# Kernel tuning notes

Measured on AMD Instinct MI355X. Metric: run time of the kernel, lower is better.

The kernel has to match this reference:

```python
import jax, jax.numpy as jnp
import numpy as np

H, D = 8, 16
HID = H * D  # hidden_channels = 128
SQRT_D = float(np.sqrt(D))


def setup_inputs() -> dict:
    key = jax.random.key(0)
    ks = iter(jax.random.split(key, 64))
    def nrm(shape, scale):
        return jax.random.normal(next(ks), shape, dtype=jnp.float32) * scale
    def rint(n, hi):
        return jax.random.randint(next(ks), (n,), 0, hi, dtype=jnp.int32)
    E = 250000
    Nh, Ni, Nt = 8000, 40000, 20000
    inp = {
        'x_herb': nrm((Nh, 400), 1.0),
        'x_ing':  nrm((Ni, 300), 1.0),
        'x_tgt':  nrm((Nt, 200), 1.0),
        # per-type input projections
        'W_herb': nrm((400, HID), 0.05), 'b_herb': jnp.zeros((HID,), jnp.float32),
        'W_ing':  nrm((300, HID), 0.06), 'b_ing':  jnp.zeros((HID,), jnp.float32),
        'W_tgt':  nrm((200, HID), 0.07), 'b_tgt':  jnp.zeros((HID,), jnp.float32),
        # HGTConv per-node-type k/q/v linears, stacked over [herb, ing, tgt]
        'Wk': nrm((3, HID, HID), 0.09), 'bk': jnp.zeros((3, HID), jnp.float32),
        'Wq': nrm((3, HID, HID), 0.09), 'bq': jnp.zeros((3, HID), jnp.float32),
        'Wv': nrm((3, HID, HID), 0.09), 'bv': jnp.zeros((3, HID), jnp.float32),
        # per-edge-type relation matrices / priors, stacked over 4 edge types
        'a_rel': nrm((4, H, D, D), 0.25),
        'm_rel': nrm((4, H, D, D), 0.25),
        'p_rel': jnp.ones((4, H), jnp.float32),
        # per-dst-node-type output linear + skip gate
        'Wa': nrm((3, HID, HID), 0.09), 'ba': jnp.zeros((3, HID), jnp.float32),
        'skip': jnp.ones((3,), jnp.float32),
        # final herb linear
        'W_out': nrm((HID, HID), 0.09), 'b_out': jnp.zeros((HID,), jnp.float32),
        # edge lists: (herb->ing contains), (ing->herb rev), (ing->tgt targets), (tgt->ing rev)
        'src_ci': rint(E, Nh), 'dst_ci': rint(E, Ni),
        'src_ic': rint(E, Ni), 'dst_ic': rint(E, Nh),
        'src_it': rint(E, Ni), 'dst_it': rint(E, Nt),
        'src_ti': rint(E, Nt), 'dst_ti': rint(E, Ni),
    }
    return inp


def _hetero_forward(x_herb, x_ing, x_tgt, W_herb, b_herb, W_ing, b_ing, W_tgt, b_tgt,
                    Wk, bk, Wq, bq, Wv, bv, a_rel, m_rel, p_rel, Wa, ba, skip,
                    W_out, b_out, src_ci, dst_ci, src_ic, dst_ic, src_it, dst_it,
                    src_ti, dst_ti):
    types = ['herb', 'ing', 'tgt']
    xs = {'herb': x_herb @ W_herb + b_herb,
          'ing':  x_ing  @ W_ing  + b_ing,
          'tgt':  x_tgt  @ W_tgt  + b_tgt}
    Ns = {t: xs[t].shape[0] for t in types}
    # per-node-type k/q/v, reshaped to [N, H, D]
    k = {t: (xs[t] @ Wk[i] + bk[i]).reshape(-1, H, D) for i, t in enumerate(types)}
    q = {t: (xs[t] @ Wq[i] + bq[i]).reshape(-1, H, D) for i, t in enumerate(types)}
    v = {t: (xs[t] @ Wv[i] + bv[i]).reshape(-1, H, D) for i, t in enumerate(types)}

    edge_defs = [  # (edge_type_id, src_type, dst_type, src_idx, dst_idx)
        (0, 'herb', 'ing', src_ci, dst_ci),
        (1, 'ing', 'herb', src_ic, dst_ic),
        (2, 'ing', 'tgt', src_it, dst_it),
        (3, 'tgt', 'ing', src_ti, dst_ti),
    ]
    contrib = {t: [] for t in types}
    for e, s, t, src, dst in edge_defs:
        # relation-specific transforms at node level, then gather per edge
        k_rel = jnp.einsum('nhd,hde->nhe', k[s], a_rel[e])  # [Ns, H, D]
        v_rel = jnp.einsum('nhd,hde->nhe', v[s], m_rel[e])  # [Ns, H, D]
        logit = (q[t][dst] * k_rel[src]).sum(-1) * (p_rel[e] / SQRT_D)  # [E, H]
        contrib[t].append((logit, v_rel[src], dst))

    out = {}
    for i, t in enumerate(types):
        logits = jnp.concatenate([c[0] for c in contrib[t]], axis=0)  # [Et, H]
        msgs = jnp.concatenate([c[1] for c in contrib[t]], axis=0)    # [Et, H, D]
        dsts = jnp.concatenate([c[2] for c in contrib[t]], axis=0)    # [Et]
        n = Ns[t]
        # segment softmax over all incoming edges of each dst node (per head)
        mx = jax.ops.segment_max(logits, dsts, num_segments=n)
        ex = jnp.exp(logits - mx[dsts])
        den = jax.ops.segment_sum(ex, dsts, num_segments=n)
        alpha = ex / (den[dsts] + 1e-16)
        agg = jax.ops.segment_sum(msgs * alpha[:, :, None], dsts, num_segments=n)
        agg = agg.reshape(n, HID)
        o = jax.nn.gelu(agg, approximate=False) @ Wa[i] + ba[i]
        g = jax.nn.sigmoid(skip[i])
        out[t] = jax.nn.relu(g * o + (1.0 - g) * xs[t])
    out_herb = out['herb'] @ W_out + b_out
    return (out_herb, out['ing'], out['tgt'])


def reference(x_herb, x_ing, x_tgt, W_herb, b_herb, W_ing, b_ing, W_tgt, b_tgt,
              Wk, bk, Wq, bq, Wv, bv, a_rel, m_rel, p_rel, Wa, ba, skip,
              W_out, b_out, src_ci, dst_ci, src_ic, dst_ic, src_it, dst_it,
              src_ti, dst_ti):
    return _hetero_forward(x_herb, x_ing, x_tgt, W_herb, b_herb, W_ing, b_ing,
                           W_tgt, b_tgt, Wk, bk, Wq, bq, Wv, bv, a_rel, m_rel,
                           p_rel, Wa, ba, skip, W_out, b_out, src_ci, dst_ci,
                           src_ic, dst_ic, src_it, dst_it, src_ti, dst_ti)
```

## Files before the change

### kernel.cpp

```cpp
#include <hip/hip_runtime.h>
#include <math.h>

#define HID 128
typedef unsigned int uint;
typedef unsigned short ushort;
typedef __attribute__((ext_vector_type(8))) short short8;
typedef __attribute__((ext_vector_type(4))) float floatx4;
typedef __attribute__((ext_vector_type(2))) float f32x2;

__device__ __forceinline__ ushort f2b(float f) {
  uint u = __float_as_uint(f);
  u += 0x7fffu + ((u >> 16) & 1u);
  return (ushort)(u >> 16);
}
__device__ __forceinline__ float b2f(ushort s) {
  return __uint_as_float(((uint)s) << 16);
}
__device__ __forceinline__ float blo(uint u) { return __uint_as_float(u << 16); }
__device__ __forceinline__ float bhi(uint u) { return __uint_as_float(u & 0xffff0000u); }
__device__ __forceinline__ f32x2 b2x2(uint u) {
  f32x2 r;
  r.x = __uint_as_float(u << 16);
  r.y = __uint_as_float(u & 0xffff0000u);
  return r;
}

__device__ __forceinline__ void gll16(const ushort* g, ushort* l) {
  __builtin_amdgcn_global_load_lds(
      (const __attribute__((address_space(1))) void*)g,
      (__attribute__((address_space(3))) void*)l, 16, 0, 0);
}

__device__ __forceinline__ size_t a_packed_us(int rr, int col) {
  int tm = rr >> 7, prow = rr & 127;
  int ptk = col >> 5, kin = col & 31;
  int sw = (kin >> 3) ^ ((prow >> 1) & 3);
  return (((size_t)tm * 4 + ptk) * 512 + (size_t)prow * 4 + sw) * 8 + (kin & 7);
}

struct PackSeg { const float* X; ushort* out; int M, K, Ktiles, start; };
struct WBlk { const float* src; ushort* dst; int K; int start; };
struct Prolog {
  PackSeg pk[3];
  int crwstart, wstart, bstart, total;
  const float *Wk, *bk, *Wv, *bv, *a_rel, *m_rel, *p_rel;
  ushort* kw_dst[4];
  ushort* vw_dst[4];
  float* bcat;
  int kb_off[4], vb_off[4];
  WBlk wb[10];
  const float* bq;
  int bq_off[3];
};

__device__ void combine_rel_elem(const Prolog& P, int idx)
{
  int col  = idx & 127;
  int rest = idx >> 7;
  int row  = rest % 129;
  rest /= 129;
  int kv = rest & 1;
  int e  = rest >> 1;
  int i  = (e + 1) >> 1;
  int h = col >> 4, j = col & 15;
  const float* Wsrc = kv ? P.Wv : P.Wk;
  const float* bsrc = kv ? P.bv : P.bk;
  const float* rel  = kv ? P.m_rel : P.a_rel;
  float acc = 0.f;
  if (row < 128) {
#pragma unroll
    for (int d = 0; d < 16; ++d)
      acc += Wsrc[(size_t)i * 16384 + (size_t)row * 128 + h * 16 + d] *
             rel[((e * 8 + h) * 16 + d) * 16 + j];
  } else {
#pragma unroll
    for (int d = 0; d < 16; ++d)
      acc += bsrc[i * 128 + h * 16 + d] * rel[((e * 8 + h) * 16 + d) * 16 + j];
  }
  if (!kv) acc *= P.p_rel[e * 8 + h] * 0.36067376022224085f;
  if (row < 128) {
    ushort* dst = kv ? P.vw_dst[e] : P.kw_dst[e];
    int tk = row >> 5, chunk = (row >> 3) & 3, m = row & 7;
    int swf = chunk ^ ((col >> 1) & 3);
    dst[((tk * 512 + col * 4 + swf) << 3) + m] = f2b(acc);
  } else {
    P.bcat[(kv ? P.vb_off[e] : P.kb_off[e]) + col] = acc;
  }
}

__device__ void conv_elem(const Prolog& P, int s0)
{
  int si = 0;
#pragma unroll
  for (int k = 1; k < 10; ++k)
    if (s0 >= P.wb[k].start) si = k;
  WBlk b = P.wb[si];
  int s = s0 - b.start;
  int tk = s >> 9, o = s & 511;
  int c = o >> 2, swf = o & 3;
  int chunk = swf ^ ((c >> 1) & 3);
  int r0 = tk * 32 + chunk * 8;
  ushort tmp[8];
#pragma unroll
  for (int m = 0; m < 8; ++m) {
    int r = r0 + m;
    tmp[m] = (r < b.K) ? f2b(b.src[(size_t)r * 128 + c]) : (ushort)0;
  }
  *(short8*)&b.dst[(size_t)s * 8] = *(short8*)tmp;
}

__global__ __launch_bounds__(256)
void prologue(Prolog P)
{
  int gtid = blockIdx.x * 256 + threadIdx.x;
  if (gtid >= P.total) return;
  if (gtid >= P.bstart) {
    int j = gtid - P.bstart;
    P.bcat[P.bq_off[j >> 7] + (j & 127)] = P.bq[j];
    return;
  }
  if (gtid >= P.wstart) { conv_elem(P, gtid - P.wstart); return; }
  if (gtid >= P.crwstart) { combine_rel_elem(P, gtid - P.crwstart); return; }
  int si = 0;
  if (gtid >= P.pk[2].start) si = 2;
  else if (gtid >= P.pk[1].start) si = 1;
  const PackSeg s = P.pk[si];
  int slot = gtid - s.start;
  int spm = s.Ktiles << 9;
  int tm = slot / spm, r2 = slot - tm * spm;
  int tk = r2 >> 9, o = r2 & 511;
  int row = o >> 2, sw = o & 3;
  int chunk = sw ^ ((row >> 1) & 3);
  int grow = tm * 128 + row;
  int gk = tk * 32 + chunk * 8;
  ushort tmp[8];
  if (grow < s.M && gk + 8 <= s.K) {
    const float* p = s.X + (size_t)grow * s.K + gk;
    float4 a = *(const float4*)p, b = *(const float4*)(p + 4);
    tmp[0] = f2b(a.x); tmp[1] = f2b(a.y); tmp[2] = f2b(a.z); tmp[3] = f2b(a.w);
    tmp[4] = f2b(b.x); tmp[5] = f2b(b.y); tmp[6] = f2b(b.z); tmp[7] = f2b(b.w);
  } else {
#pragma unroll
    for (int j = 0; j < 8; ++j) {
      int kk = gk + j;
      tmp[j] = (grow < s.M && kk < s.K) ? f2b(s.X[(size_t)grow * s.K + kk]) : (ushort)0;
    }
  }
  *(short8*)&s.out[(size_t)slot * 8] = *(short8*)tmp;
}

#define CSR_CH 1024
#define CSR_SH 9

struct EdgeStreams {
  const int* src[4]; const int* dst[4];
  int off[4]; uint rel[4]; uint ldb[4];
};

__global__ __launch_bounds__(256)
void edge_hist(EdgeStreams es, uint* __restrict__ hist, int NBs, int NBK, int E)
{
  __shared__ uint h[512];
  int b = blockIdx.x;
  int et = b / NBs;
  int i0 = (b - et * NBs) * CSR_CH;
  const int* dp = es.dst[et];
  int off = es.off[et];
  for (int t = threadIdx.x; t < NBK; t += 256) h[t] = 0;
  __syncthreads();
#pragma unroll
  for (int j = 0; j < CSR_CH / 256; ++j) {
    int idx = i0 + j * 256 + threadIdx.x;
    if (idx < E) atomicAdd(&h[(uint)(off + dp[idx]) >> CSR_SH], 1u);
  }
  __syncthreads();
  for (int t = threadIdx.x; t < NBK; t += 256)
    hist[(size_t)b * NBK + t] = h[t];
}

__global__ __launch_bounds__(256)
void bucket_scan(uint* __restrict__ hist, uint* __restrict__ bucketTot,
                 int NBlk, int NBK)
{
  __shared__ uint ws[4];
  __shared__ uint carry_s;
  int b = blockIdx.x;
  int t = threadIdx.x, lane = t & 63, w = t >> 6;
  if (t == 0) carry_s = 0;
  __syncthreads();
  for (int base = 0; base < NBlk; base += 256) {
    int i = base + t;
    uint x = (i < NBlk) ? hist[(size_t)i * NBK + b] : 0u;
    uint v = x;
#pragma unroll
    for (int o = 1; o < 64; o <<= 1) {
      uint y = __shfl_up(v, o, 64);
      if (lane >= o) v += y;
    }
    if (lane == 63) ws[w] = v;
    __syncthreads();
    uint add = carry_s;
    for (int k = 0; k < w; ++k) add += ws[k];
    if (i < NBlk) hist[(size_t)i * NBK + b] = add + v - x;
    __syncthreads();
    if (t == 255) carry_s = add + v;
    __syncthreads();
  }
  if (t == 0) bucketTot[b] = carry_s;
}

__global__ __launch_bounds__(256)
void bucket_base(const uint* __restrict__ bucketTot, uint* __restrict__ bucketBase,
                 int NBK, int* __restrict__ starts, int Ntot)
{
  __shared__ uint ws[4];
  __shared__ uint carry_s;
  int t = threadIdx.x, lane = t & 63, w = t >> 6;
  if (t == 0) carry_s = 0;
  __syncthreads();
  for (int base = 0; base < NBK; base += 256) {
    int i = base + t;
    uint x = (i < NBK) ? bucketTot[i] : 0u;
    uint v = x;
#pragma unroll
    for (int o = 1; o < 64; o <<= 1) {
      uint y = __shfl_up(v, o, 64);
      if (lane >= o) v += y;
    }
    if (lane == 63) ws[w] = v;
    __syncthreads();
    uint add = carry_s;
    for (int k = 0; k < w; ++k) add += ws[k];
    if (i < NBK) bucketBase[i] = add + v - x;
    __syncthreads();
    if (t == 255) carry_s = add + v;
    __syncthreads();
  }
  if (t == 0) { bucketBase[NBK] = carry_s; starts[Ntot] = (int)carry_s; }
}

__global__ __launch_bounds__(256)
void bucket_scatter(EdgeStreams es, const uint* __restrict__ hist,
                    const uint* __restrict__ bucketBase,
                    uint2* __restrict__ inter, int NBs, int NBK, int E)
{
  __shared__ uint cur[512];
  int b = blockIdx.x;
  int et = b / NBs;
  int i0 = (b - et * NBs) * CSR_CH;
  const int* dp = es.dst[et];
  const int* sp = es.src[et];
  int off = es.off[et];
  uint rel = es.rel[et], ldb = es.ldb[et];
  for (int t = threadIdx.x; t < NBK; t += 256)
    cur[t] = bucketBase[t] + hist[(size_t)b * NBK + t];
  __syncthreads();
#pragma unroll
  for (int j = 0; j < CSR_CH / 256; ++j) {
    int idx = i0 + j * 256 + threadIdx.x;
    if (idx < E) {
      int g = off + dp[idx];
      uint pos = atomicAdd(&cur[(uint)g >> CSR_SH], 1u);
      inter[pos] = make_uint2(rel + (uint)sp[idx] * ldb, (uint)g);
    }
  }
}

__global__ __launch_bounds__(256)
void bucket_finalize(const uint2* __restrict__ inter,
                     const uint* __restrict__ bucketBase,
                     int* __restrict__ starts, uint* __restrict__ payload, int Ntot)
{
  __shared__ uint ncnt[512];
  __shared__ uint ws[4];
  int b = blockIdx.x;
  int g0 = b << CSR_SH;
  int t = threadIdx.x, lane = t & 63, w = t >> 6;
  uint r0 = bucketBase[b], r1 = bucketBase[b + 1];
  ncnt[t] = 0; ncnt[t + 256] = 0;
  __syncthreads();
  for (uint i = r0 + t; i < r1; i += 256)
    atomicAdd(&ncnt[inter[i].y - g0], 1u);
  __syncthreads();
  uint a0 = ncnt[2 * t], a1 = ncnt[2 * t + 1];
  uint s = a0 + a1;
  uint v = s;
#pragma unroll
  for (int o = 1; o < 64; o <<= 1) {
    uint y = __shfl_up(v, o, 64);
    if (lane >= o) v += y;
  }
  if (lane == 63) ws[w] = v;
  __syncthreads();
  uint add = r0;
  for (int k = 0; k < w; ++k) add += ws[k];
  uint e0 = add + v - s;
  int gi = g0 + 2 * t;
  if (gi < Ntot)     starts[gi]     = (int)e0;
  if (gi + 1 < Ntot) starts[gi + 1] = (int)(e0 + a0);
  ncnt[2 * t] = e0;
  ncnt[2 * t + 1] = e0 + a0;
  __syncthreads();
  for (uint i = r0 + t; i < r1; i += 256) {
    uint2 rec = inter[i];
    uint pos = atomicAdd(&ncnt[rec.y - g0], 1u);
    payload[pos] = rec.x;
  }
}

struct GemmSeg {
  const ushort* A; const ushort* B; const float* bias;
  void* out; const ushort* xsP;
  int Ktiles, ldo, Mreal, skip_idx, epi, NT, start;
};
struct Gemm3 { GemmSeg s[3]; const float* skip; int nseg; };

__launch_bounds__(256)
__global__ void gemm_sched(Gemm3 g3)
{
  __shared__ __align__(16) ushort As[2][4096];
  __shared__ __align__(16) ushort Bs[2][4096];
  int bid = blockIdx.x;
  int si = 0;
  if (g3.nseg > 1 && bid >= g3.s[1].start)
    si = (g3.nseg > 2 && bid >= g3.s[2].start) ? 2 : 1;
  const GemmSeg sg = g3.s[si];
  int local = bid - sg.start;
  int tm = local / sg.NT, tn = local - tm * sg.NT;

  const int t = threadIdx.x;
  const int wave = t >> 6, lane = t & 63;
  const int wm = (wave >> 1) * 64, wn = (wave & 1) * 64;
  const int l16 = lane & 15, quad = lane >> 4;
  const int Ktiles = sg.Ktiles;

  const ushort* Abase = sg.A + (size_t)tm * Ktiles * 4096;
  const ushort* Bbase = sg.B + (size_t)tn * Ktiles * 4096;

  floatx4 acc[4][4];
#pragma unroll
  for (int i = 0; i < 4; ++i)
#pragma unroll
    for (int j = 0; j < 4; ++j) acc[i][j] = (floatx4){0.f, 0.f, 0.f, 0.f};

  auto stage = [&](int tk, int buf) {
#pragma unroll
    for (int j = 0; j < 4; ++j) {
      int c = wave * 4 + j;
      if (c < 8)
        gll16(Abase + (size_t)tk * 4096 + c * 512 + lane * 8, &As[buf][c * 512]);
      else
        gll16(Bbase + (size_t)tk * 4096 + (c - 8) * 512 + lane * 8, &Bs[buf][(c - 8) * 512]);
    }
  };

  stage(0, 0);
  __syncthreads();

  for (int tk = 0; tk < Ktiles; ++tk) {
    int buf = tk & 1;
    if (tk + 1 < Ktiles) stage(tk + 1, buf ^ 1);

    short8 af[4], bfr[4];
    const int swz = (quad ^ ((l16 >> 1) & 3)) * 8;
#pragma unroll
    for (int i = 0; i < 4; ++i) {
      af[i]  = *(const short8*)&As[buf][(wm + i * 16 + l16) * 32 + swz];
      bfr[i] = *(const short8*)&Bs[buf][(wn + i * 16 + l16) * 32 + swz];
    }
#pragma unroll
    for (int mi = 0; mi < 4; ++mi)
#pragma unroll
      for (int ni = 0; ni < 4; ++ni)
        acc[mi][ni] = __builtin_amdgcn_mfma_f32_16x16x32_bf16(
            af[mi], bfr[ni], acc[mi][ni], 0, 0, 0);
    __syncthreads();
  }

  const int epi = sg.epi;
  float g = 0.f, omg = 0.f;
  if (epi == 2 || epi == 3) {
    float s = g3.skip[sg.skip_idx];
    g = 1.f / (1.f + __expf(-s));
    omg = 1.f - g;
  }
#pragma unroll
  for (int ni = 0; ni < 4; ++ni) {
    int col = tn * 128 + wn + ni * 16 + l16;
    float bb = sg.bias[col];
#pragma unroll
    for (int mi = 0; mi < 4; ++mi) {
      int rloc = wm + mi * 16 + quad * 4;
#pragma unroll
      for (int r = 0; r < 4; ++r) {
        int prow = rloc + r;
        int rr = tm * 128 + prow;
        float v = acc[mi][ni][r] + bb;
        if (epi == 0) {
          ((ushort*)sg.out)[(size_t)rr * sg.ldo + col] = f2b(v);
        } else if (epi == 1) {
          if (rr < sg.Mreal) ((float*)sg.out)[(size_t)rr * sg.ldo + col] = v;
        } else if (epi == 2) {
          if (rr < sg.Mreal) {
            float xo = b2f(sg.xsP[a_packed_us(rr, col)]);
            ((float*)sg.out)[(size_t)rr * sg.ldo + col] = fmaxf(g * v + omg * xo, 0.f);
          }
        } else if (epi == 3) {
          float xo = b2f(sg.xsP[a_packed_us(rr, col)]);
          ((ushort*)sg.out)[a_packed_us(rr, col)] = f2b(fmaxf(g * v + omg * xo, 0.f));
        } else {
          ((ushort*)sg.out)[a_packed_us(rr, col)] = f2b(v);
        }
      }
    }
  }
}

struct GatherType { const ushort* q; ushort* agg; int ldq; };
struct GatherDesc { GatherType ty[3]; int n0, n1; };

__launch_bounds__(256)
__global__ void gather_all(const int* __restrict__ starts,
                           const uint* __restrict__ payload,
                           const ushort* __restrict__ kvbase,
                           GatherDesc gd, int Ntot)
{
  int wid = (blockIdx.x * 256 + threadIdx.x) >> 6;
  if (wid >= Ntot) return;
  int lane = threadIdx.x & 63;
  int g = lane >> 4, l = lane & 15;

  GatherType T;
  int d;
  if (wid < gd.n0)      { T = gd.ty[0]; d = wid; }
  else if (wid < gd.n1) { T = gd.ty[1]; d = wid - gd.n0; }
  else                  { T = gd.ty[2]; d = wid - gd.n1; }

  const char* kvb = (const char*)kvbase;
  const uint lofs = (uint)l * 16u;

  uint4 qv = *(const uint4*)(T.q + (size_t)d * T.ldq + l * 8);
  f32x2 q0 = b2x2(qv.x), q1 = b2x2(qv.y), q2 = b2x2(qv.z), q3 = b2x2(qv.w);

  int e0 = starts[wid], e1 = starts[wid + 1];
  float lsum = 0.f;
  f32x2 ac0 = {0.f, 0.f}, ac1 = {0.f, 0.f}, ac2 = {0.f, 0.f}, ac3 = {0.f, 0.f};

  for (int eb = e0; eb < e1; eb += 8) {
    int eA = eb + g, eB = eA + 4;
    bool actA = eA < e1, actB = eB < e1;
    uint pA = payload[actA ? eA : e0];
    uint pB = payload[actB ? eB : e0];
    const char* bA = kvb + (pA + lofs);
    const char* bB = kvb + (pB + lofs);
    uint4 kA = *(const uint4*)bA;
    uint4 vA = *(const uint4*)(bA + 256);
    uint4 kB = *(const uint4*)bB;
    uint4 vB = *(const uint4*)(bB + 256);

    f32x2 dA = q0 * b2x2(kA.x);
    dA = __builtin_elementwise_fma(q1, b2x2(kA.y), dA);
    dA = __builtin_elementwise_fma(q2, b2x2(kA.z), dA);
    dA = __builtin_elementwise_fma(q3, b2x2(kA.w), dA);
    f32x2 dB = q0 * b2x2(kB.x);
    dB = __builtin_elementwise_fma(q1, b2x2(kB.y), dB);
    dB = __builtin_elementwise_fma(q2, b2x2(kB.z), dB);
    dB = __builtin_elementwise_fma(q3, b2x2(kB.w), dB);
    float pa = dA.x + dA.y;
    float pb = dB.x + dB.y;
    pa += __shfl_xor(pa, 1, 64);
    pb += __shfl_xor(pb, 1, 64);
    float exA = exp2f(fminf(pa, 115.4f));
    float exB = exp2f(fminf(pb, 115.4f));
    exA = actA ? exA : 0.f;
    exB = actB ? exB : 0.f;
    lsum += exA + exB;
    f32x2 xA = {exA, exA}, xB = {exB, exB};
    ac0 = __builtin_elementwise_fma(xA, b2x2(vA.x), ac0);
    ac1 = __builtin_elementwise_fma(xA, b2x2(vA.y), ac1);
    ac2 = __builtin_elementwise_fma(xA, b2x2(vA.z), ac2);
    ac3 = __builtin_elementwise_fma(xA, b2x2(vA.w), ac3);
    ac0 = __builtin_elementwise_fma(xB, b2x2(vB.x), ac0);
    ac1 = __builtin_elementwise_fma(xB, b2x2(vB.y), ac1);
    ac2 = __builtin_elementwise_fma(xB, b2x2(vB.z), ac2);
    ac3 = __builtin_elementwise_fma(xB, b2x2(vB.w), ac3);
  }

  float s0 = ac0.x, s1 = ac0.y, s2 = ac1.x, s3 = ac1.y;
  float s4 = ac2.x, s5 = ac2.y, s6 = ac3.x, s7 = ac3.y;
#define MRG(v) v += __shfl_xor(v, 16, 64); v += __shfl_xor(v, 32, 64)
  MRG(lsum); MRG(s0); MRG(s1); MRG(s2); MRG(s3); MRG(s4); MRG(s5); MRG(s6); MRG(s7);
#undef MRG

  float inv = 1.f / (lsum + 1e-16f);
  float m0 = (g & 1) ? s2 : s0, m1 = (g & 1) ? s6 : s4;
  float n0 = (g & 1) ? s3 : s1, n1 = (g & 1) ? s7 : s5;
  float x0 = ((g & 2) ? m1 : m0) * inv;
  float x1 = ((g & 2) ? n1 : n0) * inv;
  float g0 = 0.5f * x0 * (1.f + erff(x0 * 0.70710678118654752f));
  float g1 = 0.5f * x1 * (1.f + erff(x1 * 0.70710678118654752f));
  int tm = d >> 7, row = d & 127;
  int tk = l >> 2, sw = (l & 3) ^ ((row >> 1) & 3);
  size_t us = (((size_t)tm * 4 + tk) * 512 + (size_t)row * 4 + sw) * 8 + 2 * g;
  *(uint*)(T.agg + us) = ((uint)f2b(g1) << 16) | (uint)f2b(g0);
}

extern "C" void kernel_launch(void* const* d_in, const int* in_sizes, int n_in,
                              void* d_out, int out_size, void* d_ws, size_t ws_size,
                              hipStream_t stream)
{
  const float* x_herb = (const float*)d_in[0];
  const float* x_ing  = (const float*)d_in[1];
  const float* x_tgt  = (const float*)d_in[2];
  const float* W_herb = (const float*)d_in[3];
  const float* b_herb = (const float*)d_in[4];
  const float* W_ing  = (const float*)d_in[5];
  const float* b_ing  = (const float*)d_in[6];
  const float* W_tgt  = (const float*)d_in[7];
  const float* b_tgt  = (const float*)d_in[8];
  const float* Wk     = (const float*)d_in[9];
  const float* bk     = (const float*)d_in[10];
  const float* Wq     = (const float*)d_in[11];
  const float* bq     = (const float*)d_in[12];
  const float* Wv     = (const float*)d_in[13];
  const float* bv     = (const float*)d_in[14];
  const float* a_rel  = (const float*)d_in[15];
  const float* m_rel  = (const float*)d_in[16];
  const float* p_rel  = (const float*)d_in[17];
  const float* Wa     = (const float*)d_in[18];
  const float* ba     = (const float*)d_in[19];
  const float* skip   = (const float*)d_in[20];
  const float* W_out  = (const float*)d_in[21];
  const float* b_out  = (const float*)d_in[22];
  const int* srcs[4] = {(const int*)d_in[23], (const int*)d_in[25],
                        (const int*)d_in[27], (const int*)d_in[29]};
  const int* dsts[4] = {(const int*)d_in[24], (const int*)d_in[26],
                        (const int*)d_in[28], (const int*)d_in[30]};

  const int Nh = in_sizes[0] / 400;
  const int Ni = in_sizes[1] / 300;
  const int Nt = in_sizes[2] / 200;
  const int E  = in_sizes[23];
  const int Ntot = Nh + Ni + Nt;

  const int MT_h = (Nh + 127) / 128, MT_i = (Ni + 127) / 128, MT_t = (Nt + 127) / 128;
  const int KT_h = 13, KT_i = 10, KT_t = 7;

  const int NBs = (E + CSR_CH - 1) / CSR_CH;
  const int NBlk = 4 * NBs;
  const int NBK = (Ntot + (1 << CSR_SH) - 1) >> CSR_SH;

  char* base = (char*)d_ws;
  size_t off = 0;
  auto A = [&](size_t bytes) -> void* {
    void* p = base + off; off += (bytes + 255) & ~(size_t)255; return p;
  };
  ushort* xp_h  = (ushort*)A((size_t)MT_h * KT_h * 8192);
  ushort* xp_i  = (ushort*)A((size_t)MT_i * KT_i * 8192);
  ushort* xp_t  = (ushort*)A((size_t)MT_t * KT_t * 8192);
  ushort* xsP_h = (ushort*)A((size_t)MT_h * 4 * 8192);
  ushort* xsP_i = (ushort*)A((size_t)MT_i * 4 * 8192);
  ushort* xsP_t = (ushort*)A((size_t)MT_t * 4 * 8192);
  ushort* fused_h = (ushort*)A((size_t)MT_h * 128 * 384 * 2);
  ushort* fused_i = (ushort*)A((size_t)MT_i * 128 * 640 * 2);
  ushort* fused_t = (ushort*)A((size_t)MT_t * 128 * 384 * 2);
  ushort* aggp_h  = (ushort*)A((size_t)MT_h * 4 * 8192);
  ushort* aggp_i  = (ushort*)A((size_t)MT_i * 4 * 8192);
  ushort* aggp_t  = (ushort*)A((size_t)MT_t * 4 * 8192);
  ushort* htmp_p  = (ushort*)A((size_t)MT_h * 4 * 8192);
  ushort* Weff1_h = (ushort*)A((size_t)KT_h * 8192);
  ushort* Weff1_i = (ushort*)A((size_t)KT_i * 8192);
  ushort* Weff1_t = (ushort*)A((size_t)KT_t * 8192);
  ushort* Wcat_h = (ushort*)A((size_t)3 * 4 * 8192);
  ushort* Wcat_i = (ushort*)A((size_t)5 * 4 * 8192);
  ushort* Wcat_t = (ushort*)A((size_t)3 * 4 * 8192);
  float* bcat   = (float*)A(1408 * 4);
  ushort* Wa_t   = (ushort*)A((size_t)3 * 16384 * 2);
  ushort* Wout_t = (ushort*)A((size_t)16384 * 2);
  int* starts  = (int*)A((size_t)(Ntot + 4) * 4);
  uint* payload = (uint*)A((size_t)(4 * E + 8) * 4);
  uint* hist    = (uint*)A((size_t)NBlk * NBK * 4);
  uint* bucketTot  = (uint*)A((size_t)NBK * 4);
  uint* bucketBase = (uint*)A((size_t)(NBK + 1) * 4);
  uint2* inter  = (uint2*)A((size_t)(4 * E + 8) * 8);
  (void)ws_size; (void)n_in;

  const int toff_h = 0, toff_i = Nh, toff_t = Nh + Ni;
  dim3 blk(256);

  int sl_h = MT_h * KT_h * 512, sl_i = MT_i * KT_i * 512, sl_t = MT_t * KT_t * 512;
  Prolog P;
  P.pk[0] = {x_herb, xp_h, Nh, 400, KT_h, 0};
  P.pk[1] = {x_ing,  xp_i, Ni, 300, KT_i, sl_h};
  P.pk[2] = {x_tgt,  xp_t, Nt, 200, KT_t, sl_h + sl_i};
  P.crwstart = sl_h + sl_i + sl_t;
  P.wstart = P.crwstart + 4 * 2 * 129 * 128;
  {
    const float* wsrc10[10] = {W_herb, W_ing, W_tgt, Wq, Wq + 16384, Wq + 32768,
                               Wa, Wa + 16384, Wa + 32768, W_out};
    ushort* wdst10[10] = {Weff1_h, Weff1_i, Weff1_t, Wcat_h, Wcat_i, Wcat_t,
                          Wa_t, Wa_t + 16384, Wa_t + 32768, Wout_t};
    int wk10[10] = {400, 300, 200, 128, 128, 128, 128, 128, 128, 128};
    int wcum = 0;
    for (int z = 0; z < 10; ++z) {
      P.wb[z] = {wsrc10[z], wdst10[z], wk10[z], wcum};
      wcum += ((wk10[z] + 31) / 32) * 512;
    }
    P.bstart = P.wstart + wcum;
  }
  P.total = P.bstart + 384;
  P.Wk = Wk; P.bk = bk; P.Wv = Wv; P.bv = bv;
  P.a_rel = a_rel; P.m_rel = m_rel; P.p_rel = p_rel;
  P.kw_dst[0] = Wcat_h + 16384; P.vw_dst[0] = Wcat_h + 32768;
  P.kw_dst[1] = Wcat_i + 16384; P.vw_dst[1] = Wcat_i + 32768;
  P.kw_dst[2] = Wcat_i + 49152; P.vw_dst[2] = Wcat_i + 65536;
  P.kw_dst[3] = Wcat_t + 16384; P.vw_dst[3] = Wcat_t + 32768;
  P.bcat = bcat;
  P.kb_off[0] = 128;  P.vb_off[0] = 256;
  P.kb_off[1] = 512;  P.vb_off[1] = 640;
  P.kb_off[2] = 768;  P.vb_off[2] = 896;
  P.kb_off[3] = 1152; P.vb_off[3] = 1280;
  P.bq = bq;
  P.bq_off[0] = 0; P.bq_off[1] = 384; P.bq_off[2] = 1024;
  prologue<<<(P.total + 255) / 256, blk, 0, stream>>>(P);

  uint fi2 = (uint)((size_t)(fused_i - fused_h) * 2);
  uint ft2 = (uint)((size_t)(fused_t - fused_h) * 2);
  EdgeStreams ES;
  ES.src[0] = srcs[0]; ES.dst[0] = dsts[0]; ES.off[0] = toff_i;
  ES.rel[0] = 256u;        ES.ldb[0] = 768u;
  ES.src[1] = srcs[1]; ES.dst[1] = dsts[1]; ES.off[1] = toff_h;
  ES.rel[1] = fi2 + 256u;  ES.ldb[1] = 1280u;
  ES.src[2] = srcs[2]; ES.dst[2] = dsts[2]; ES.off[2] = toff_t;
  ES.rel[2] = fi2 + 768u;  ES.ldb[2] = 1280u;
  ES.src[3] = srcs[3]; ES.dst[3] = dsts[3]; ES.off[3] = toff_i;
  ES.rel[3] = ft2 + 256u;  ES.ldb[3] = 768u;
  edge_hist<<<NBlk, blk, 0, stream>>>(ES, hist, NBs, NBK, E);
  bucket_scan<<<NBK, blk, 0, stream>>>(hist, bucketTot, NBlk, NBK);
  bucket_base<<<1, blk, 0, stream>>>(bucketTot, bucketBase, NBK, starts, Ntot);
  bucket_scatter<<<NBlk, blk, 0, stream>>>(ES, hist, bucketBase, inter, NBs, NBK, E);
  bucket_finalize<<<NBK, blk, 0, stream>>>(inter, bucketBase, starts, payload, Ntot);

  Gemm3 G1;
  G1.skip = skip; G1.nseg = 3;
  G1.s[0] = {xp_h, Weff1_h, b_herb, xsP_h, nullptr, KT_h, 0, 0, 0, 4, 1, 0};
  G1.s[1] = {xp_i, Weff1_i, b_ing,  xsP_i, nullptr, KT_i, 0, 0, 0, 4, 1, MT_h};
  G1.s[2] = {xp_t, Weff1_t, b_tgt,  xsP_t, nullptr, KT_t, 0, 0, 0, 4, 1, MT_h + MT_i};
  gemm_sched<<<MT_h + MT_i + MT_t, blk, 0, stream>>>(G1);

  Gemm3 G2;
  G2.skip = skip; G2.nseg = 3;
  G2.s[0] = {xsP_h, Wcat_h, bcat + 0,    fused_h, nullptr, 4, 384, 0, 0, 0, 3, 0};
  G2.s[1] = {xsP_i, Wcat_i, bcat + 384,  fused_i, nullptr, 4, 640, 0, 0, 0, 5, MT_h * 3};
  G2.s[2] = {xsP_t, Wcat_t, bcat + 1024, fused_t, nullptr, 4, 384, 0, 0, 0, 3,
             MT_h * 3 + MT_i * 5};
  gemm_sched<<<MT_h * 3 + MT_i * 5 + MT_t * 3, blk, 0, stream>>>(G2);

  GatherDesc GD;
  GD.n0 = Nh; GD.n1 = Nh + Ni;
  GD.ty[0] = {fused_h, aggp_h, 384};
  GD.ty[1] = {fused_i, aggp_i, 640};
  GD.ty[2] = {fused_t, aggp_t, 384};
  gather_all<<<(Ntot + 3) / 4, blk, 0, stream>>>(starts, payload, fused_h, GD, Ntot);

  float* outp = (float*)d_out;
  float* out_herb = outp;
  float* out_ing  = outp + (size_t)Nh * HID;
  float* out_tgt  = outp + (size_t)(Nh + Ni) * HID;
  Gemm3 GE;
  GE.skip = skip; GE.nseg = 3;
  GE.s[0] = {aggp_h, Wa_t + 0 * 16384, ba + 0 * 128, htmp_p, xsP_h,
             4, 0, 0, 0, 3, 1, 0};
  GE.s[1] = {aggp_i, Wa_t + 1 * 16384, ba + 1 * 128, out_ing, xsP_i,
             4, 128, Ni, 1, 2, 1, MT_h};
  GE.s[2] = {aggp_t, Wa_t + 2 * 16384, ba + 2 * 128, out_tgt, xsP_t,
             4, 128, Nt, 2, 2, 1, MT_h + MT_i};
  gemm_sched<<<MT_h + MT_i + MT_t, blk, 0, stream>>>(GE);

  Gemm3 GF;
  GF.skip = skip; GF.nseg = 1;
  GF.s[0] = {htmp_p, Wout_t, b_out, out_herb, nullptr, 4, 128, Nh, 0, 1, 1, 0};
  GF.s[1] = GF.s[0]; GF.s[2] = GF.s[0];
  gemm_sched<<<MT_h, blk, 0, stream>>>(GF);
  (void)out_size;
}
```

Before: 456.4 us.

## Fold edge histogram into prologue, drop bucket_base kernel, unroll gather loop

```diff
diff --git a/kernel.cpp b/kernel.cpp
--- a/kernel.cpp
+++ b/kernel.cpp
@@ -37,6 +37,14 @@
   int sw = (kin >> 3) ^ ((prow >> 1) & 3);
   return (((size_t)tm * 4 + ptk) * 512 + (size_t)prow * 4 + sw) * 8 + (kin & 7);
 }
+
+#define CSR_CH 2048
+#define CSR_SH 9
+
+struct EdgeStreams {
+  const int* src[4]; const int* dst[4];
+  int off[4]; uint rel[4]; uint ldb[4];
+};
 
 struct PackSeg { const float* X; ushort* out; int M, K, Ktiles, start; };
 struct WBlk { const float* src; ushort* dst; int K; int start; };
@@ -51,6 +59,10 @@
   WBlk wb[10];
   const float* bq;
   int bq_off[3];
+  const int* edst[4];
+  int eoff[4];
+  uint* hist;
+  int NBs, NBH, NBK, E;
 };
 
 __device__ void combine_rel_elem(const Prolog& P, int idx)
@@ -112,7 +124,26 @@
 __global__ __launch_bounds__(256)
 void prologue(Prolog P)
 {
-  int gtid = blockIdx.x * 256 + threadIdx.x;
+  __shared__ uint h[512];
+  int bI = blockIdx.x;
+  if (bI < P.NBH) {
+    int et = bI / P.NBs;
+    int i0 = (bI - et * P.NBs) * CSR_CH;
+    const int* dp = P.edst[et];
+    int off = P.eoff[et];
+    for (int t = threadIdx.x; t < P.NBK; t += 256) h[t] = 0;
+    __syncthreads();
+#pragma unroll
+    for (int j = 0; j < CSR_CH / 256; ++j) {
+      int idx = i0 + j * 256 + threadIdx.x;
+      if (idx < P.E) atomicAdd(&h[(uint)(off + dp[idx]) >> CSR_SH], 1u);
+    }
+    __syncthreads();
+    for (int t = threadIdx.x; t < P.NBK; t += 256)
+      P.hist[(size_t)t * P.NBH + bI] = h[t];
+    return;
+  }
+  int gtid = (bI - P.NBH) * 256 + threadIdx.x;
   if (gtid >= P.total) return;
   if (gtid >= P.bstart) {
     int j = gtid - P.bstart;
@@ -149,38 +180,8 @@
   *(short8*)&s.out[(size_t)slot * 8] = *(short8*)tmp;
 }
 
-#define CSR_CH 1024
-#define CSR_SH 9
-
-struct EdgeStreams {
-  const int* src[4]; const int* dst[4];
-  int off[4]; uint rel[4]; uint ldb[4];
-};
-
 __global__ __launch_bounds__(256)
-void edge_hist(EdgeStreams es, uint* __restrict__ hist, int NBs, int NBK, int E)
-{
-  __shared__ uint h[512];
-  int b = blockIdx.x;
-  int et = b / NBs;
-  int i0 = (b - et * NBs) * CSR_CH;
-  const int* dp = es.dst[et];
-  int off = es.off[et];
-  for (int t = threadIdx.x; t < NBK; t += 256) h[t] = 0;
-  __syncthreads();
-#pragma unroll
-  for (int j = 0; j < CSR_CH / 256; ++j) {
-    int idx = i0 + j * 256 + threadIdx.x;
-    if (idx < E) atomicAdd(&h[(uint)(off + dp[idx]) >> CSR_SH], 1u);
-  }
-  __syncthreads();
-  for (int t = threadIdx.x; t < NBK; t += 256)
-    hist[(size_t)b * NBK + t] = h[t];
-}
-
-__global__ __launch_bounds__(256)
-void bucket_scan(uint* __restrict__ hist, uint* __restrict__ bucketTot,
-                 int NBlk, int NBK)
+void bucket_scan(uint* __restrict__ hist, uint* __restrict__ bucketTot, int NBH)
 {
   __shared__ uint ws[4];
   __shared__ uint carry_s;
@@ -188,9 +189,9 @@
   int t = threadIdx.x, lane = t & 63, w = t >> 6;
   if (t == 0) carry_s = 0;
   __syncthreads();
-  for (int base = 0; base < NBlk; base += 256) {
+  for (int base = 0; base < NBH; base += 256) {
     int i = base + t;
-    uint x = (i < NBlk) ? hist[(size_t)i * NBK + b] : 0u;
+    uint x = (i < NBH) ? hist[(size_t)b * NBH + i] : 0u;
     uint v = x;
 #pragma unroll
     for (int o = 1; o < 64; o <<= 1) {
@@ -201,7 +202,7 @@
     __syncthreads();
     uint add = carry_s;
     for (int k = 0; k < w; ++k) add += ws[k];
-    if (i < NBlk) hist[(size_t)i * NBK + b] = add + v - x;
+    if (i < NBH) hist[(size_t)b * NBH + i] = add + v - x;
     __syncthreads();
     if (t == 255) carry_s = add + v;
     __syncthreads();
@@ -209,42 +210,40 @@
   if (t == 0) bucketTot[b] = carry_s;
 }
 
-__global__ __launch_bounds__(256)
-void bucket_base(const uint* __restrict__ bucketTot, uint* __restrict__ bucketBase,
-                 int NBK, int* __restrict__ starts, int Ntot)
-{
-  __shared__ uint ws[4];
-  __shared__ uint carry_s;
+__device__ __forceinline__ void base_scan(const uint* __restrict__ bucketTot,
+                                          uint* sb, uint* ws, int NBK)
+{
   int t = threadIdx.x, lane = t & 63, w = t >> 6;
-  if (t == 0) carry_s = 0;
-  __syncthreads();
-  for (int base = 0; base < NBK; base += 256) {
-    int i = base + t;
-    uint x = (i < NBK) ? bucketTot[i] : 0u;
-    uint v = x;
-#pragma unroll
-    for (int o = 1; o < 64; o <<= 1) {
-      uint y = __shfl_up(v, o, 64);
-      if (lane >= o) v += y;
-    }
-    if (lane == 63) ws[w] = v;
-    __syncthreads();
-    uint add = carry_s;
-    for (int k = 0; k < w; ++k) add += ws[k];
-    if (i < NBK) bucketBase[i] = add + v - x;
-    __syncthreads();
-    if (t == 255) carry_s = add + v;
-    __syncthreads();
-  }
-  if (t == 0) { bucketBase[NBK] = carry_s; starts[Ntot] = (int)carry_s; }
+  sb[t] = (t < NBK) ? bucketTot[t] : 0u;
+  sb[t + 256] = (t + 256 < NBK) ? bucketTot[t + 256] : 0u;
+  __syncthreads();
+  uint a0 = sb[2 * t], a1 = sb[2 * t + 1];
+  uint s = a0 + a1;
+  uint v = s;
+#pragma unroll
+  for (int o = 1; o < 64; o <<= 1) {
+    uint y = __shfl_up(v, o, 64);
+    if (lane >= o) v += y;
+  }
+  if (lane == 63) ws[w] = v;
+  __syncthreads();
+  uint add = 0;
+  for (int k = 0; k < w; ++k) add += ws[k];
+  uint e0 = add + v - s;
+  sb[2 * t] = e0;
+  sb[2 * t + 1] = e0 + a0;
+  __syncthreads();
 }
 
 __global__ __launch_bounds__(256)
 void bucket_scatter(EdgeStreams es, const uint* __restrict__ hist,
-                    const uint* __restrict__ bucketBase,
-                    uint2* __restrict__ inter, int NBs, int NBK, int E)
-{
+                    const uint* __restrict__ bucketTot,
+                    uint2* __restrict__ inter, int NBs, int NBH, int NBK, int E)
+{
+  __shared__ uint sb[516];
+  __shared__ uint ws[4];
   __shared__ uint cur[512];
+  base_scan(bucketTot, sb, ws, NBK);
   int b = blockIdx.x;
   int et = b / NBs;
   int i0 = (b - et * NBs) * CSR_CH;
@@ -253,7 +252,7 @@
   int off = es.off[et];
   uint rel = es.rel[et], ldb = es.ldb[et];
   for (int t = threadIdx.x; t < NBK; t += 256)
-    cur[t] = bucketBase[t] + hist[(size_t)b * NBK + t];
+    cur[t] = sb[t] + hist[(size_t)t * NBH + b];
   __syncthreads();
 #pragma unroll
   for (int j = 0; j < CSR_CH / 256; ++j) {
@@ -268,15 +267,19 @@
 
 __global__ __launch_bounds__(256)
 void bucket_finalize(const uint2* __restrict__ inter,
-                     const uint* __restrict__ bucketBase,
-                     int* __restrict__ starts, uint* __restrict__ payload, int Ntot)
-{
+                     const uint* __restrict__ bucketTot,
+                     int* __restrict__ starts, uint* __restrict__ payload,
+                     int Ntot, int NBK)
+{
+  __shared__ uint sb[516];
   __shared__ uint ncnt[512];
   __shared__ uint ws[4];
+  base_scan(bucketTot, sb, ws, NBK);
   int b = blockIdx.x;
   int g0 = b << CSR_SH;
   int t = threadIdx.x, lane = t & 63, w = t >> 6;
-  uint r0 = bucketBase[b], r1 = bucketBase[b + 1];
+  uint r0 = sb[b], r1 = sb[b + 1];
+  if (b == NBK - 1 && t == 0) starts[Ntot] = (int)r1;
   ncnt[t] = 0; ncnt[t + 256] = 0;
   __syncthreads();
   for (uint i = r0 + t; i < r1; i += 256)
@@ -436,8 +439,7 @@
   else if (wid < gd.n1) { T = gd.ty[1]; d = wid - gd.n0; }
   else                  { T = gd.ty[2]; d = wid - gd.n1; }
 
-  const char* kvb = (const char*)kvbase;
-  const uint lofs = (uint)l * 16u;
+  const char* kvl = (const char*)kvbase + l * 16;
 
   uint4 qv = *(const uint4*)(T.q + (size_t)d * T.ldq + l * 8);
   f32x2 q0 = b2x2(qv.x), q1 = b2x2(qv.y), q2 = b2x2(qv.z), q3 = b2x2(qv.w);
@@ -446,44 +448,43 @@
   float lsum = 0.f;
   f32x2 ac0 = {0.f, 0.f}, ac1 = {0.f, 0.f}, ac2 = {0.f, 0.f}, ac3 = {0.f, 0.f};
 
-  for (int eb = e0; eb < e1; eb += 8) {
-    int eA = eb + g, eB = eA + 4;
-    bool actA = eA < e1, actB = eB < e1;
-    uint pA = payload[actA ? eA : e0];
-    uint pB = payload[actB ? eB : e0];
-    const char* bA = kvb + (pA + lofs);
-    const char* bB = kvb + (pB + lofs);
-    uint4 kA = *(const uint4*)bA;
-    uint4 vA = *(const uint4*)(bA + 256);
-    uint4 kB = *(const uint4*)bB;
-    uint4 vB = *(const uint4*)(bB + 256);
-
-    f32x2 dA = q0 * b2x2(kA.x);
-    dA = __builtin_elementwise_fma(q1, b2x2(kA.y), dA);
-    dA = __builtin_elementwise_fma(q2, b2x2(kA.z), dA);
-    dA = __builtin_elementwise_fma(q3, b2x2(kA.w), dA);
-    f32x2 dB = q0 * b2x2(kB.x);
-    dB = __builtin_elementwise_fma(q1, b2x2(kB.y), dB);
-    dB = __builtin_elementwise_fma(q2, b2x2(kB.z), dB);
-    dB = __builtin_elementwise_fma(q3, b2x2(kB.w), dB);
-    float pa = dA.x + dA.y;
-    float pb = dB.x + dB.y;
-    pa += __shfl_xor(pa, 1, 64);
-    pb += __shfl_xor(pb, 1, 64);
-    float exA = exp2f(fminf(pa, 115.4f));
-    float exB = exp2f(fminf(pb, 115.4f));
-    exA = actA ? exA : 0.f;
-    exB = actB ? exB : 0.f;
-    lsum += exA + exB;
-    f32x2 xA = {exA, exA}, xB = {exB, exB};
-    ac0 = __builtin_elementwise_fma(xA, b2x2(vA.x), ac0);
-    ac1 = __builtin_elementwise_fma(xA, b2x2(vA.y), ac1);
-    ac2 = __builtin_elementwise_fma(xA, b2x2(vA.z), ac2);
-    ac3 = __builtin_elementwise_fma(xA, b2x2(vA.w), ac3);
-    ac0 = __builtin_elementwise_fma(xB, b2x2(vB.x), ac0);
-    ac1 = __builtin_elementwise_fma(xB, b2x2(vB.y), ac1);
-    ac2 = __builtin_elementwise_fma(xB, b2x2(vB.z), ac2);
-    ac3 = __builtin_elementwise_fma(xB, b2x2(vB.w), ac3);
+  for (int eb = e0; eb < e1; eb += 16) {
+    uint p[4];
+    bool act[4];
+#pragma unroll
+    for (int b = 0; b < 4; ++b) {
+      int e = eb + g + 4 * b;
+      act[b] = e < e1;
+      p[b] = payload[act[b] ? e : e0];
+    }
+    uint4 kk[4], vv[4];
+#pragma unroll
+    for (int b = 0; b < 4; ++b) {
+      const char* ba = kvl + p[b];
+      kk[b] = *(const uint4*)ba;
+      vv[b] = *(const uint4*)(ba + 256);
+    }
+    float ex[4];
+#pragma unroll
+    for (int b = 0; b < 4; ++b) {
+      f32x2 dA = q0 * b2x2(kk[b].x);
+      dA = __builtin_elementwise_fma(q1, b2x2(kk[b].y), dA);
+      dA = __builtin_elementwise_fma(q2, b2x2(kk[b].z), dA);
+      dA = __builtin_elementwise_fma(q3, b2x2(kk[b].w), dA);
+      float pa = dA.x + dA.y;
+      pa += __shfl_xor(pa, 1, 64);
+      float t2 = exp2f(fminf(pa, 115.4f));
+      ex[b] = act[b] ? t2 : 0.f;
+    }
+    lsum += (ex[0] + ex[1]) + (ex[2] + ex[3]);
+#pragma unroll
+    for (int b = 0; b < 4; ++b) {
+      f32x2 xb = {ex[b], ex[b]};
+      ac0 = __builtin_elementwise_fma(xb, b2x2(vv[b].x), ac0);
+      ac1 = __builtin_elementwise_fma(xb, b2x2(vv[b].y), ac1);
+      ac2 = __builtin_elementwise_fma(xb, b2x2(vv[b].z), ac2);
+      ac3 = __builtin_elementwise_fma(xb, b2x2(vv[b].w), ac3);
+    }
   }
 
   float s0 = ac0.x, s1 = ac0.y, s2 = ac1.x, s3 = ac1.y;
@@ -547,7 +548,7 @@
   const int KT_h = 13, KT_i = 10, KT_t = 7;
 
   const int NBs = (E + CSR_CH - 1) / CSR_CH;
-  const int NBlk = 4 * NBs;
+  const int NBH = 4 * NBs;
   const int NBK = (Ntot + (1 << CSR_SH) - 1) >> CSR_SH;
 
   char* base = (char*)d_ws;
@@ -579,14 +580,16 @@
   ushort* Wout_t = (ushort*)A((size_t)16384 * 2);
   int* starts  = (int*)A((size_t)(Ntot + 4) * 4);
   uint* payload = (uint*)A((size_t)(4 * E + 8) * 4);
-  uint* hist    = (uint*)A((size_t)NBlk * NBK * 4);
+  uint* hist    = (uint*)A((size_t)NBK * NBH * 4);
   uint* bucketTot  = (uint*)A((size_t)NBK * 4);
-  uint* bucketBase = (uint*)A((size_t)(NBK + 1) * 4);
   uint2* inter  = (uint2*)A((size_t)(4 * E + 8) * 8);
   (void)ws_size; (void)n_in;
 
   const int toff_h = 0, toff_i = Nh, toff_t = Nh + Ni;
   dim3 blk(256);
+
+  uint fi2 = (uint)((size_t)(fused_i - fused_h) * 2);
+  uint ft2 = (uint)((size_t)(fused_t - fused_h) * 2);
 
   int sl_h = MT_h * KT_h * 512, sl_i = MT_i * KT_i * 512, sl_t = MT_t * KT_t * 512;
   Prolog P;
@@ -622,10 +625,13 @@
   P.kb_off[3] = 1152; P.vb_off[3] = 1280;
   P.bq = bq;
   P.bq_off[0] = 0; P.bq_off[1] = 384; P.bq_off[2] = 1024;
-  prologue<<<(P.total + 255) / 256, blk, 0, stream>>>(P);
-
-  uint fi2 = (uint)((size_t)(fused_i - fused_h) * 2);
-  uint ft2 = (uint)((size_t)(fused_t - fused_h) * 2);
+  P.edst[0] = dsts[0]; P.eoff[0] = toff_i;
+  P.edst[1] = dsts[1]; P.eoff[1] = toff_h;
+  P.edst[2] = dsts[2]; P.eoff[2] = toff_t;
+  P.edst[3] = dsts[3]; P.eoff[3] = toff_i;
+  P.hist = hist; P.NBs = NBs; P.NBH = NBH; P.NBK = NBK; P.E = E;
+  prologue<<<NBH + (P.total + 255) / 256, blk, 0, stream>>>(P);
+
   EdgeStreams ES;
   ES.src[0] = srcs[0]; ES.dst[0] = dsts[0]; ES.off[0] = toff_i;
   ES.rel[0] = 256u;        ES.ldb[0] = 768u;
@@ -635,11 +641,9 @@
   ES.rel[2] = fi2 + 768u;  ES.ldb[2] = 1280u;
   ES.src[3] = srcs[3]; ES.dst[3] = dsts[3]; ES.off[3] = toff_i;
   ES.rel[3] = ft2 + 256u;  ES.ldb[3] = 768u;
-  edge_hist<<<NBlk, blk, 0, stream>>>(ES, hist, NBs, NBK, E);
-  bucket_scan<<<NBK, blk, 0, stream>>>(hist, bucketTot, NBlk, NBK);
-  bucket_base<<<1, blk, 0, stream>>>(bucketTot, bucketBase, NBK, starts, Ntot);
-  bucket_scatter<<<NBlk, blk, 0, stream>>>(ES, hist, bucketBase, inter, NBs, NBK, E);
-  bucket_finalize<<<NBK, blk, 0, stream>>>(inter, bucketBase, starts, payload, Ntot);
+  bucket_scan<<<NBK, blk, 0, stream>>>(hist, bucketTot, NBH);
+  bucket_scatter<<<NBH, blk, 0, stream>>>(ES, hist, bucketTot, inter, NBs, NBH, NBK, E);
+  bucket_finalize<<<NBK, blk, 0, stream>>>(inter, bucketTot, starts, payload, Ntot, NBK);
 
   Gemm3 G1;
   G1.skip = skip; G1.nseg = 3;
```

Result: no change. 460.7 us (+0.9%).
